# Kernel tuning notes

Hardware: AMD Instinct MI355X
Metric: run time of the kernel (lower is better)

## Reference

```python
import jax, jax.numpy as jnp
import numpy as np

NUM_FEATURES = 1024
NUM_SAMPLES = 32768
BATCH = 4096
TEMP = 0.05
EPS = 1e-12


def setup_inputs() -> dict:
    key = jax.random.key(0)
    k1, k2, k3, k4 = jax.random.split(key, 4)
    inputs = jax.random.normal(k1, (BATCH, NUM_FEATURES), dtype=jnp.float32)
    targets = jax.random.randint(k2, (BATCH,), 0, NUM_SAMPLES, dtype=jnp.int64)
    corrected_targets = jax.random.randint(k3, (BATCH,), 0, NUM_SAMPLES, dtype=jnp.int64)
    # memory bank: buffer is zeros-initialized in torch, but in practice it is
    # filled with L2-normalized cluster centroids before use; emulate that.
    feats = jax.random.normal(k4, (NUM_SAMPLES, NUM_FEATURES), dtype=jnp.float32)
    feats = feats / jnp.linalg.norm(feats, axis=1, keepdims=True)
    return {"inputs": inputs, "targets": targets,
            "corrected_targets": corrected_targets, "features": feats}


def reference(inputs, targets, corrected_targets, features):
    # F.normalize(inputs, dim=1)
    x = inputs / jnp.maximum(jnp.linalg.norm(inputs, axis=1, keepdims=True), EPS)
    # CM.forward: inputs @ features.T, then / temp
    logits = jnp.einsum('bd,nd->bn', x, features) / TEMP  # [B, N]
    # F.cross_entropy(logits, corrected_targets, reduction='mean')
    logp = jax.nn.log_softmax(logits, axis=1)
    nll = -jnp.take_along_axis(logp, corrected_targets[:, None], axis=1)[:, 0]
    return jnp.mean(nll)
```

## Files before the change

### kernel.cpp

```cpp
#include <hip/hip_runtime.h>
#include <stdint.h>

#define B_ROWS 4096
#define N_FEAT 32768
#define K_DIM  1024
#define BM 256
#define BN 256
#define NT2 (N_FEAT / BN)
#define NKT (K_DIM / 64)

typedef __attribute__((ext_vector_type(8))) short bf16x8;
typedef __attribute__((ext_vector_type(4))) float f32x4;
typedef __attribute__((address_space(1))) unsigned char ga_u8;
typedef __attribute__((address_space(3))) unsigned char lds_u8;

__device__ inline unsigned short f2bf(float f) {
  union { float f; unsigned u; } v; v.f = f;
  unsigned r = v.u + 0x7FFF + ((v.u >> 16) & 1);
  return (unsigned short)(r >> 16);
}
__device__ inline float bf2f(unsigned short u) {
  union { unsigned u; float f; } v; v.u = ((unsigned)u) << 16;
  return v.f;
}

__global__ void k_norm(const float* __restrict__ in, unsigned short* __restrict__ xbf) {
  int row = blockIdx.x;
  int t = threadIdx.x;
  float4 v = reinterpret_cast<const float4*>(in + (size_t)row * K_DIM)[t];
  float ssq = v.x * v.x + v.y * v.y + v.z * v.z + v.w * v.w;
  #pragma unroll
  for (int d = 1; d < 64; d <<= 1) ssq += __shfl_xor(ssq, d);
  __shared__ float sm[4];
  if ((t & 63) == 0) sm[t >> 6] = ssq;
  __syncthreads();
  float nrm = sqrtf(sm[0] + sm[1] + sm[2] + sm[3]);
  float inv = 1.0f / fmaxf(nrm, 1e-12f);
  ushort4 o;
  o.x = f2bf(v.x * inv); o.y = f2bf(v.y * inv);
  o.z = f2bf(v.z * inv); o.w = f2bf(v.w * inv);
  reinterpret_cast<ushort4*>(xbf + (size_t)row * K_DIM)[t] = o;
}

__global__ void k_conv(const float* __restrict__ f, unsigned short* __restrict__ fbf, long n4) {
  long i = blockIdx.x * (long)blockDim.x + threadIdx.x;
  long stride = (long)gridDim.x * blockDim.x;
  for (; i < n4; i += stride) {
    float4 v = reinterpret_cast<const float4*>(f)[i];
    ushort4 o;
    o.x = f2bf(v.x); o.y = f2bf(v.y); o.z = f2bf(v.z); o.w = f2bf(v.w);
    reinterpret_cast<ushort4*>(fbf)[i] = o;
  }
}

__global__ void k_tgt(const unsigned short* __restrict__ xbf,
                      const unsigned short* __restrict__ fbf,
                      const int* __restrict__ tgt, float* __restrict__ out) {
  int row = blockIdx.x * 4 + (threadIdx.x >> 6);
  int lane = threadIdx.x & 63;
  int t = tgt[row];
  const uint4* xa = reinterpret_cast<const uint4*>(xbf + (size_t)row * K_DIM + lane * 16);
  const uint4* fa = reinterpret_cast<const uint4*>(fbf + (size_t)t * K_DIM + lane * 16);
  float s = 0.f;
  #pragma unroll
  for (int j = 0; j < 2; ++j) {
    uint4 av = xa[j], fv = fa[j];
    const unsigned* ap = &av.x;
    const unsigned* fp = &fv.x;
    #pragma unroll
    for (int q = 0; q < 4; ++q) {
      s += bf2f((unsigned short)(ap[q] & 0xffff)) * bf2f((unsigned short)(fp[q] & 0xffff));
      s += bf2f((unsigned short)(ap[q] >> 16)) * bf2f((unsigned short)(fp[q] >> 16));
    }
  }
  #pragma unroll
  for (int d = 1; d < 64; d <<= 1) s += __shfl_xor(s, d);
  if (lane == 0) out[row] = s * 20.0f;
}


#define XSTR(s) STR(s)
#define STR(s) #s
#define WAITV(N)  asm volatile("s_waitcnt vmcnt(" XSTR(N) ")" ::: "memory")
#define LGKM0     do { asm volatile("s_waitcnt lgkmcnt(0)" ::: "memory"); __builtin_amdgcn_sched_barrier(0); } while(0)
#define BAR       __builtin_amdgcn_s_barrier()
#define SCHED0    __builtin_amdgcn_sched_barrier(0)
#define PRIO1     __builtin_amdgcn_s_setprio(1)
#define PRIO0     __builtin_amdgcn_s_setprio(0)

__launch_bounds__(512, 2)
__global__ void k_gemm8(const unsigned short* __restrict__ xbf,
                        const unsigned short* __restrict__ fbf,
                        float* __restrict__ m_part, float* __restrict__ l_part) {
  __shared__ __align__(16) char lds_all[131072];
  char* ldsc = lds_all;

  int tid = threadIdx.x;
  int lane = tid & 63;
  int wid = tid >> 6;
  int wr = wid >> 2;
  int wc = wid & 3;
  int r15 = lane & 15;
  int g = lane >> 4;

  int bid = blockIdx.x;
  int swz = (bid & 7) * 256 + (bid >> 3);
  int mt = swz >> 7;
  int nt = swz & 127;
  int mBase = mt * BM, nBase = nt * BN;

  int lswz = ((g ^ ((r15 >> 1) & 3)) << 4);
  int aRow = (wr * 128 + r15) * 64 + lswz;
  int bRow = (wc * 64 + r15) * 64 + lswz + 32768;

  int stRow = wid * 32 + (lane >> 2);
  int src_cb = (((lane & 3) ^ ((lane >> 3) & 3)) << 4);
  const char* srcA = (const char*)xbf + (size_t)(mBase + stRow) * (K_DIM * 2) + src_cb;
  const char* srcB = (const char*)fbf + (size_t)(nBase + stRow) * (K_DIM * 2) + src_cb;

#define STAGE(BSEL_, MAT, KH, T) do { \
    const char* gsrc = ((MAT) ? srcB : srcA) + (T) * 128 + (KH) * 64; \
    char* ldst = ldsc + (BSEL_) * 65536 + (MAT) * 32768 + (KH) * 16384 + wid * 2048; \
    __builtin_amdgcn_global_load_lds((const ga_u8*)gsrc, (lds_u8*)ldst, 16, 0, 0); \
    __builtin_amdgcn_global_load_lds((const ga_u8*)(gsrc + 32768), (lds_u8*)(ldst + 1024), 16, 0, 0); \
  } while(0)

#define LDA(Q, KH, BUFC) do { \
    _Pragma("unroll") \
    for (int fm = 0; fm < 4; ++fm) \
      a[fm] = *reinterpret_cast<const bf16x8*>((BUFC) + (KH) * 16384 + aRow + (Q) * 4096 + fm * 1024); \
  } while(0)

#define LDB(KH, BUFC) do { \
    _Pragma("unroll") \
    for (int fn = 0; fn < 4; ++fn) \
      b[fn] = *reinterpret_cast<const bf16x8*>((BUFC) + (KH) * 16384 + bRow + fn * 1024); \
  } while(0)

#define MM(Q) do { \
    _Pragma("unroll") \
    for (int fm = 0; fm < 4; ++fm) \
      _Pragma("unroll") \
      for (int fn = 0; fn < 4; ++fn) \
        acc[(Q) * 4 + fm][fn] = __builtin_amdgcn_mfma_f32_16x16x32_bf16(a[fm], b[fn], acc[(Q) * 4 + fm][fn], 0, 0, 0); \
  } while(0)

#define TILE(T, ISS1, ISS2, VMA, VMB) do { \
    int bs = (T) & 1; \
    char* bufc = ldsc + bs * 65536; \
     \
    LDA(0, 0, bufc); LDB(0, bufc); \
    if (ISS1) { STAGE(((T) + 1) & 1, 0, 1, (T) + 1); } \
    BAR; LGKM0; PRIO1; MM(0); PRIO0; BAR; SCHED0; \
     \
    LDA(1, 0, bufc); \
    if (ISS1) { STAGE(((T) + 1) & 1, 1, 1, (T) + 1); } \
    WAITV(VMA); \
    BAR; LGKM0; PRIO1; MM(1); PRIO0; BAR; SCHED0; \
     \
    LDA(0, 1, bufc); LDB(1, bufc); \
    if (ISS2) { STAGE(bs, 0, 0, (T) + 2); } \
    BAR; LGKM0; PRIO1; MM(0); PRIO0; BAR; SCHED0; \
     \
    LDA(1, 1, bufc); \
    if (ISS2) { STAGE(bs, 1, 0, (T) + 2); } \
    WAITV(VMB); \
    BAR; LGKM0; PRIO1; MM(1); PRIO0; BAR; SCHED0; \
  } while(0)

  f32x4 acc[8][4];
  #pragma unroll
  for (int i = 0; i < 8; ++i)
    #pragma unroll
    for (int j = 0; j < 4; ++j)
      acc[i][j] = (f32x4){0.f, 0.f, 0.f, 0.f};
  bf16x8 a[4], b[4];

  STAGE(0, 0, 0, 0); STAGE(0, 1, 0, 0);
  STAGE(0, 0, 1, 0); STAGE(0, 1, 1, 0);
  STAGE(1, 0, 0, 1); STAGE(1, 1, 0, 1);
  WAITV(8);
  BAR; SCHED0;

  for (int t = 0; t < NKT - 2; ++t) {
    TILE(t, 1, 1, 8, 8);
  }
  TILE(14, 1, 0, 8, 4);
  TILE(15, 0, 0, 0, 0);

  asm volatile("s_waitcnt vmcnt(0) lgkmcnt(0)" ::: "memory");
  __syncthreads();
  float* sm_m = (float*)lds_all;
  float* sm_l = (float*)(lds_all + 4096);

  #pragma unroll
  for (int mf = 0; mf < 8; ++mf)
    #pragma unroll
    for (int fn = 0; fn < 4; ++fn)
      acc[mf][fn] = acc[mf][fn] * 20.0f;

  #pragma unroll
  for (int mf = 0; mf < 8; ++mf) {
    #pragma unroll
    for (int reg = 0; reg < 4; ++reg) {
      float mx = -1e30f;
      #pragma unroll
      for (int fn = 0; fn < 4; ++fn) mx = fmaxf(mx, acc[mf][fn][reg]);
      mx = fmaxf(mx, __shfl_xor(mx, 1));
      mx = fmaxf(mx, __shfl_xor(mx, 2));
      mx = fmaxf(mx, __shfl_xor(mx, 4));
      mx = fmaxf(mx, __shfl_xor(mx, 8));
      float sum = 0.f;
      #pragma unroll
      for (int fn = 0; fn < 4; ++fn) sum += __expf(acc[mf][fn][reg] - mx);
      sum += __shfl_xor(sum, 1);
      sum += __shfl_xor(sum, 2);
      sum += __shfl_xor(sum, 4);
      sum += __shfl_xor(sum, 8);
      if ((lane & 15) == 0) {
        int r = wr * 128 + mf * 16 + (lane >> 4) * 4 + reg;
        sm_m[wc * 256 + r] = mx;
        sm_l[wc * 256 + r] = sum;
      }
    }
  }
  __syncthreads();
  if (tid < 256) {
    float M = sm_m[tid], L = sm_l[tid];
    #pragma unroll
    for (int w = 1; w < 4; ++w) {
      float mo = sm_m[w * 256 + tid], lo = sm_l[w * 256 + tid];
      float mn = fmaxf(M, mo);
      L = L * __expf(M - mn) + lo * __expf(mo - mn);
      M = mn;
    }
    size_t idx = (size_t)(mBase + tid) * NT2 + nt;
    m_part[idx] = M;
    l_part[idx] = L;
  }
}

__global__ void k_comb(const float* __restrict__ m_part, const float* __restrict__ l_part,
                       const float* __restrict__ tgt_logit, float* __restrict__ nll) {
  int row = blockIdx.x;
  int lane = threadIdx.x;
  size_t base = (size_t)row * NT2;
  float m = m_part[base + lane];
  float l = l_part[base + lane];
  float m2 = m_part[base + 64 + lane];
  float l2 = l_part[base + 64 + lane];
  float mn = fmaxf(m, m2);
  l = l * __expf(m - mn) + l2 * __expf(m2 - mn);
  m = mn;
  #pragma unroll
  for (int d = 1; d < 64; d <<= 1) {
    float mo = __shfl_xor(m, d);
    float lo = __shfl_xor(l, d);
    float mx = fmaxf(m, mo);
    l = l * __expf(m - mx) + lo * __expf(mo - mx);
    m = mx;
  }
  if (lane == 0) nll[row] = m + __logf(l) - tgt_logit[row];
}

__global__ void k_mean(const float* __restrict__ nll, float* __restrict__ out) {
  int t = threadIdx.x;
  float s = 0.f;
  for (int i = t; i < B_ROWS; i += 256) s += nll[i];
  #pragma unroll
  for (int d = 1; d < 64; d <<= 1) s += __shfl_xor(s, d);
  __shared__ float sm[4];
  if ((t & 63) == 0) sm[t >> 6] = s;
  __syncthreads();
  if (t == 0) out[0] = (sm[0] + sm[1] + sm[2] + sm[3]) * (1.0f / B_ROWS);
}

extern "C" void kernel_launch(void* const* d_in, const int* in_sizes, int n_in,
                              void* d_out, int out_size, void* d_ws, size_t ws_size,
                              hipStream_t stream) {
  const float* inputs = (const float*)d_in[0];
  const int* ctgt = (const int*)d_in[2];
  const float* feats = (const float*)d_in[3];
  float* out = (float*)d_out;

  char* ws = (char*)d_ws;
  unsigned short* xbf = (unsigned short*)ws;
  unsigned short* fbf = (unsigned short*)(ws + (8ull << 20));
  float* m_part = (float*)(ws + (72ull << 20));
  float* l_part = (float*)(ws + (74ull << 20));
  float* tgt_logit = (float*)(ws + (76ull << 20));
  float* nll = (float*)(ws + (76ull << 20) + (64ull << 10));

  k_norm<<<B_ROWS, 256, 0, stream>>>(inputs, xbf);
  k_conv<<<2048, 256, 0, stream>>>(feats, fbf, (long)N_FEAT * K_DIM / 4);
  k_tgt<<<B_ROWS / 4, 256, 0, stream>>>(xbf, fbf, ctgt, tgt_logit);
  k_gemm8<<<(B_ROWS / BM) * (N_FEAT / BN), 512, 0, stream>>>(xbf, fbf, m_part, l_part);
  k_comb<<<B_ROWS, 64, 0, stream>>>(m_part, l_part, tgt_logit, nll);
  k_mean<<<1, 256, 0, stream>>>(nll, out);
}
```

Before: 521.8 us.

## Merge prep kernels, fold mean into combine via atomics, restructure GEMM phases

Fuses the input-normalize and feature-convert kernels into one launch, and replaces the separate mean kernel with an atomicAdd in the combine kernel after a memset. The GEMM inner loop is restructured from four half-M sub-phases per K tile into two full-M phases that load all 8 A fragments at once and issue both A and B stages together. This cuts launch count and barriers, at the cost of more live registers for A fragments and a nondeterministic float summation order.

```diff
diff --git a/kernel.cpp b/kernel.cpp
--- a/kernel.cpp
+++ b/kernel.cpp
@@ -24,32 +24,35 @@
   return v.f;
 }
 
-__global__ void k_norm(const float* __restrict__ in, unsigned short* __restrict__ xbf) {
-  int row = blockIdx.x;
+__global__ void k_prep(const float* __restrict__ in, unsigned short* __restrict__ xbf,
+                       const float* __restrict__ f, unsigned short* __restrict__ fbf) {
+  int bid = blockIdx.x;
   int t = threadIdx.x;
-  float4 v = reinterpret_cast<const float4*>(in + (size_t)row * K_DIM)[t];
-  float ssq = v.x * v.x + v.y * v.y + v.z * v.z + v.w * v.w;
-  #pragma unroll
-  for (int d = 1; d < 64; d <<= 1) ssq += __shfl_xor(ssq, d);
-  __shared__ float sm[4];
-  if ((t & 63) == 0) sm[t >> 6] = ssq;
-  __syncthreads();
-  float nrm = sqrtf(sm[0] + sm[1] + sm[2] + sm[3]);
-  float inv = 1.0f / fmaxf(nrm, 1e-12f);
-  ushort4 o;
-  o.x = f2bf(v.x * inv); o.y = f2bf(v.y * inv);
-  o.z = f2bf(v.z * inv); o.w = f2bf(v.w * inv);
-  reinterpret_cast<ushort4*>(xbf + (size_t)row * K_DIM)[t] = o;
-}
-
-__global__ void k_conv(const float* __restrict__ f, unsigned short* __restrict__ fbf, long n4) {
-  long i = blockIdx.x * (long)blockDim.x + threadIdx.x;
-  long stride = (long)gridDim.x * blockDim.x;
-  for (; i < n4; i += stride) {
-    float4 v = reinterpret_cast<const float4*>(f)[i];
+  if (bid < B_ROWS) {
+    int row = bid;
+    float4 v = reinterpret_cast<const float4*>(in + (size_t)row * K_DIM)[t];
+    float ssq = v.x * v.x + v.y * v.y + v.z * v.z + v.w * v.w;
+    #pragma unroll
+    for (int d = 1; d < 64; d <<= 1) ssq += __shfl_xor(ssq, d);
+    __shared__ float sm[4];
+    if ((t & 63) == 0) sm[t >> 6] = ssq;
+    __syncthreads();
+    float nrm = sqrtf(sm[0] + sm[1] + sm[2] + sm[3]);
+    float inv = 1.0f / fmaxf(nrm, 1e-12f);
     ushort4 o;
-    o.x = f2bf(v.x); o.y = f2bf(v.y); o.z = f2bf(v.z); o.w = f2bf(v.w);
-    reinterpret_cast<ushort4*>(fbf)[i] = o;
+    o.x = f2bf(v.x * inv); o.y = f2bf(v.y * inv);
+    o.z = f2bf(v.z * inv); o.w = f2bf(v.w * inv);
+    reinterpret_cast<ushort4*>(xbf + (size_t)row * K_DIM)[t] = o;
+  } else {
+    const long n4 = (long)N_FEAT * K_DIM / 4;
+    long i = (long)(bid - B_ROWS) * 256 + t;
+    const long stride = 2048L * 256;
+    for (; i < n4; i += stride) {
+      float4 v = reinterpret_cast<const float4*>(f)[i];
+      ushort4 o;
+      o.x = f2bf(v.x); o.y = f2bf(v.y); o.z = f2bf(v.z); o.w = f2bf(v.w);
+      reinterpret_cast<ushort4*>(fbf)[i] = o;
+    }
   }
 }
 
@@ -125,47 +128,23 @@
     __builtin_amdgcn_global_load_lds((const ga_u8*)(gsrc + 32768), (lds_u8*)(ldst + 1024), 16, 0, 0); \
   } while(0)
 
-#define LDA(Q, KH, BUFC) do { \
+#define PHASE(T, KH, DOST, SB, SKH, ST, VMN) do { \
+    char* bufc = ldsc + ((T) & 1) * 65536 + (KH) * 16384; \
     _Pragma("unroll") \
-    for (int fm = 0; fm < 4; ++fm) \
-      a[fm] = *reinterpret_cast<const bf16x8*>((BUFC) + (KH) * 16384 + aRow + (Q) * 4096 + fm * 1024); \
-  } while(0)
-
-#define LDB(KH, BUFC) do { \
+    for (int fm = 0; fm < 8; ++fm) \
+      a[fm] = *reinterpret_cast<const bf16x8*>(bufc + aRow + fm * 1024); \
     _Pragma("unroll") \
     for (int fn = 0; fn < 4; ++fn) \
-      b[fn] = *reinterpret_cast<const bf16x8*>((BUFC) + (KH) * 16384 + bRow + fn * 1024); \
-  } while(0)
-
-#define MM(Q) do { \
+      b[fn] = *reinterpret_cast<const bf16x8*>(bufc + bRow + fn * 1024); \
+    if (DOST) { STAGE(SB, 0, SKH, ST); STAGE(SB, 1, SKH, ST); } \
+    WAITV(VMN); \
+    BAR; LGKM0; PRIO1; \
     _Pragma("unroll") \
-    for (int fm = 0; fm < 4; ++fm) \
+    for (int fm = 0; fm < 8; ++fm) \
       _Pragma("unroll") \
       for (int fn = 0; fn < 4; ++fn) \
-        acc[(Q) * 4 + fm][fn] = __builtin_amdgcn_mfma_f32_16x16x32_bf16(a[fm], b[fn], acc[(Q) * 4 + fm][fn], 0, 0, 0); \
-  } while(0)
-
-#define TILE(T, ISS1, ISS2, VMA, VMB) do { \
-    int bs = (T) & 1; \
-    char* bufc = ldsc + bs * 65536; \
-     \
-    LDA(0, 0, bufc); LDB(0, bufc); \
-    if (ISS1) { STAGE(((T) + 1) & 1, 0, 1, (T) + 1); } \
-    BAR; LGKM0; PRIO1; MM(0); PRIO0; BAR; SCHED0; \
-     \
-    LDA(1, 0, bufc); \
-    if (ISS1) { STAGE(((T) + 1) & 1, 1, 1, (T) + 1); } \
-    WAITV(VMA); \
-    BAR; LGKM0; PRIO1; MM(1); PRIO0; BAR; SCHED0; \
-     \
-    LDA(0, 1, bufc); LDB(1, bufc); \
-    if (ISS2) { STAGE(bs, 0, 0, (T) + 2); } \
-    BAR; LGKM0; PRIO1; MM(0); PRIO0; BAR; SCHED0; \
-     \
-    LDA(1, 1, bufc); \
-    if (ISS2) { STAGE(bs, 1, 0, (T) + 2); } \
-    WAITV(VMB); \
-    BAR; LGKM0; PRIO1; MM(1); PRIO0; BAR; SCHED0; \
+        acc[fm][fn] = __builtin_amdgcn_mfma_f32_16x16x32_bf16(a[fm], b[fn], acc[fm][fn], 0, 0, 0); \
+    PRIO0; BAR; SCHED0; \
   } while(0)
 
   f32x4 acc[8][4];
@@ -174,7 +153,7 @@
     #pragma unroll
     for (int j = 0; j < 4; ++j)
       acc[i][j] = (f32x4){0.f, 0.f, 0.f, 0.f};
-  bf16x8 a[4], b[4];
+  bf16x8 a[8], b[4];
 
   STAGE(0, 0, 0, 0); STAGE(0, 1, 0, 0);
   STAGE(0, 0, 1, 0); STAGE(0, 1, 1, 0);
@@ -183,10 +162,13 @@
   BAR; SCHED0;
 
   for (int t = 0; t < NKT - 2; ++t) {
-    TILE(t, 1, 1, 8, 8);
-  }
-  TILE(14, 1, 0, 8, 4);
-  TILE(15, 0, 0, 0, 0);
+    PHASE(t, 0, 1, (t + 1) & 1, 1, t + 1, 8);
+    PHASE(t, 1, 1, t & 1,       0, t + 2, 8);
+  }
+  PHASE(14, 0, 1, 1, 1, 15, 8);
+  PHASE(14, 1, 0, 0, 0, 0, 4);
+  PHASE(15, 0, 0, 0, 0, 0, 0);
+  PHASE(15, 1, 0, 0, 0, 0, 0);
 
   asm volatile("s_waitcnt vmcnt(0) lgkmcnt(0)" ::: "memory");
   __syncthreads();
@@ -241,7 +223,7 @@
 }
 
 __global__ void k_comb(const float* __restrict__ m_part, const float* __restrict__ l_part,
-                       const float* __restrict__ tgt_logit, float* __restrict__ nll) {
+                       const float* __restrict__ tgt_logit, float* __restrict__ out) {
   int row = blockIdx.x;
   int lane = threadIdx.x;
   size_t base = (size_t)row * NT2;
@@ -260,19 +242,10 @@
     l = l * __expf(m - mx) + lo * __expf(mo - mx);
     m = mx;
   }
-  if (lane == 0) nll[row] = m + __logf(l) - tgt_logit[row];
-}
-
-__global__ void k_mean(const float* __restrict__ nll, float* __restrict__ out) {
-  int t = threadIdx.x;
-  float s = 0.f;
-  for (int i = t; i < B_ROWS; i += 256) s += nll[i];
-  #pragma unroll
-  for (int d = 1; d < 64; d <<= 1) s += __shfl_xor(s, d);
-  __shared__ float sm[4];
-  if ((t & 63) == 0) sm[t >> 6] = s;
-  __syncthreads();
-  if (t == 0) out[0] = (sm[0] + sm[1] + sm[2] + sm[3]) * (1.0f / B_ROWS);
+  if (lane == 0) {
+    float nll = m + __logf(l) - tgt_logit[row];
+    atomicAdd(out, nll * (1.0f / B_ROWS));
+  }
 }
 
 extern "C" void kernel_launch(void* const* d_in, const int* in_sizes, int n_in,
@@ -289,12 +262,10 @@
   float* m_part = (float*)(ws + (72ull << 20));
   float* l_part = (float*)(ws + (74ull << 20));
   float* tgt_logit = (float*)(ws + (76ull << 20));
-  float* nll = (float*)(ws + (76ull << 20) + (64ull << 10));
-
-  k_norm<<<B_ROWS, 256, 0, stream>>>(inputs, xbf);
-  k_conv<<<2048, 256, 0, stream>>>(feats, fbf, (long)N_FEAT * K_DIM / 4);
+
+  hipMemsetAsync(out, 0, sizeof(float), stream);
+  k_prep<<<B_ROWS + 2048, 256, 0, stream>>>(inputs, xbf, feats, fbf);
   k_tgt<<<B_ROWS / 4, 256, 0, stream>>>(xbf, fbf, ctgt, tgt_logit);
   k_gemm8<<<(B_ROWS / BM) * (N_FEAT / BN), 512, 0, stream>>>(xbf, fbf, m_part, l_part);
-  k_comb<<<B_ROWS, 64, 0, stream>>>(m_part, l_part, tgt_logit, nll);
-  k_mean<<<1, 256, 0, stream>>>(nll, out);
-}
+  k_comb<<<B_ROWS, 64, 0, stream>>>(m_part, l_part, tgt_logit, out);
+}
```

Result: slower. 599.0 us (+14.8%).
